# Performance work log

Hardware: AMD Instinct MI355X
Metric: run time of the kernel (lower is better)

Reference implementation:

```python
import jax, jax.numpy as jnp
import numpy as np

ALPHA = 1.0
BETA = 10.0
MARGIN = 0.5


def setup_inputs() -> dict:
    key = jax.random.key(0)
    k1, k2 = jax.random.split(key)
    emb = jax.random.normal(k1, (4096, 512), dtype=jnp.float32)
    # module docstring: embeddings are L2-normalized
    emb = emb / jnp.linalg.norm(emb, axis=1, keepdims=True)
    labels = jax.random.randint(k2, (4096,), 0, 64, dtype=jnp.int64)
    return {"embeddings": emb, "labels": labels}


def reference(embeddings, labels):
    n = embeddings.shape[0]
    sim = embeddings @ embeddings.T  # [n, n]
    labels_eq = labels[None, :] == labels[:, None]
    eye = jnp.eye(n, dtype=bool)
    pos_mask = labels_eq & ~eye
    neg_mask = ~labels_eq & ~eye

    # masked exp-sums (masked entries contribute 0, matching torch's
    # clone/NEG_INF/zero-out dance without materializing extra copies)
    pos_exp = jnp.where(pos_mask, jnp.exp(-ALPHA * (sim - MARGIN)), 0.0)
    neg_exp = jnp.where(neg_mask, jnp.exp(BETA * (sim - MARGIN)), 0.0)
    pos_term = (1.0 / ALPHA) * jnp.log1p(pos_exp.sum(axis=1))
    neg_term = (1.0 / BETA) * jnp.log1p(neg_exp.sum(axis=1))

    valid = pos_mask.any(axis=1) & neg_mask.any(axis=1)
    n_valid = valid.sum()
    total = jnp.where(valid, pos_term + neg_term, 0.0).sum()
    return jnp.where(n_valid > 0, total / jnp.maximum(n_valid, 1).astype(sim.dtype), 0.0)
```

## Files before the change

### kernel.cpp

```cpp
#include <hip/hip_runtime.h>
#include <hip/hip_bf16.h>

#define N 4096
#define D 512
#define MARGIN 0.5f
#define BETA 10.0f

typedef __attribute__((ext_vector_type(8))) short short8;
typedef __attribute__((ext_vector_type(4))) float floatx4;

__device__ inline unsigned short f2bf(float f) {
    unsigned u = __float_as_uint(f);
    u += 0x7fffu + ((u >> 16) & 1u);
    return (unsigned short)(u >> 16);
}

#define GLOAD_LDS16(gp, lp)                                             \
    __builtin_amdgcn_global_load_lds(                                   \
        (const __attribute__((address_space(1))) void*)(gp),            \
        (__attribute__((address_space(3))) void*)(lp), 16, 0, 0)

__global__ __launch_bounds__(256) void convert_bf16_kernel(
        const float4* __restrict__ in, ushort4* __restrict__ out,
        float* __restrict__ sums ) {
    int idx = blockIdx.x * 256 + threadIdx.x;
    if (idx < 2 * N) sums[idx] = 0.f;
    float4 v = in[idx];
    ushort4 o;
    o.x = f2bf(v.x); o.y = f2bf(v.y); o.z = f2bf(v.z); o.w = f2bf(v.w);
    out[idx] = o;
}

__global__ __launch_bounds__(256, 4) void ms_loss_gemm(
        const unsigned short* __restrict__ Ebf,
        const int* __restrict__ labels,
        float* __restrict__ pos_sum,
        float* __restrict__ neg_sum) {
    __shared__ char Als[64 * 256];
    __shared__ char Bls[64 * 256];
    __shared__ int rlab[64];
    __shared__ int clab[64];

    int t = blockIdx.x;
    int bi = 0;
    while (t >= (64 - bi)) { t -= (64 - bi); ++bi; }
    const int bj = bi + t;
    const bool diag = (bi == bj);

    const int tid  = threadIdx.x;
    const int wave = tid >> 6;
    const int lane = tid & 63;
    const int quad = lane >> 4;
    const int lcol = lane & 15;
    const int wrow = wave >> 1;
    const int wcol = wave & 1;
    const int ibase = bi * 64;
    const int jbase = bj * 64;

    if (tid < 64)        rlab[tid]      = labels[ibase + tid];
    else if (tid < 128)  clab[tid - 64] = labels[jbase + tid - 64];

    floatx4 acc[2][2];
#pragma unroll
    for (int mt = 0; mt < 2; ++mt)
#pragma unroll
        for (int nt = 0; nt < 2; ++nt)
            acc[mt][nt] = (floatx4){0.f, 0.f, 0.f, 0.f};

    const char* Eb = (const char*)Ebf;
    const int srow = lane >> 4;
    const int sgrp = wave * 4 + srow;
    const int sck  = ((lane & 15) ^ sgrp) * 16;
    const size_t aoff0 = (size_t)(ibase + sgrp) * 1024 + sck;
    const size_t boff0 = (size_t)(jbase + sgrp) * 1024 + sck;
    const int ldso = wave * 1024 + lane * 16;

#define STAGE(kt_)                                                         \
    {                                                                      \
        const int kb_ = (kt_) * 256;                                       \
        _Pragma("unroll")                                                  \
        for (int it = 0; it < 4; ++it) {                                   \
            GLOAD_LDS16(Eb + aoff0 + (size_t)it * 16384 + kb_,             \
                        Als + ldso + it * 4096);                           \
            if (!diag)                                                     \
                GLOAD_LDS16(Eb + boff0 + (size_t)it * 16384 + kb_,         \
                            Bls + ldso + it * 4096);                       \
        }                                                                  \
    }

#pragma unroll
    for (int kt = 0; kt < D / 128; ++kt) {
        __syncthreads();
        STAGE(kt);
        __syncthreads();

        const char* Ac = Als;
        const char* Bc = diag ? Als : Bls;
#pragma unroll
        for (int s = 0; s < 4; ++s) {
            short8 a[2], b[2];
            const int rslot = ((s * 4 + quad) ^ lcol) * 16;
#pragma unroll
            for (int mt = 0; mt < 2; ++mt) {
                int r = wrow * 32 + mt * 16 + lcol;
                a[mt] = *(const short8*)(Ac + r * 256 + rslot);
            }
#pragma unroll
            for (int nt = 0; nt < 2; ++nt) {
                int c = wcol * 32 + nt * 16 + lcol;
                b[nt] = *(const short8*)(Bc + c * 256 + rslot);
            }
#pragma unroll
            for (int mt = 0; mt < 2; ++mt)
#pragma unroll
                for (int nt = 0; nt < 2; ++nt)
                    acc[mt][nt] = __builtin_amdgcn_mfma_f32_16x16x32_bf16(
                        a[mt], b[nt], acc[mt][nt], 0, 0, 0);
        }
    }

    int ljv[2], gjv[2];
#pragma unroll
    for (int nt = 0; nt < 2; ++nt) {
        int cl = wcol * 32 + nt * 16 + lcol;
        ljv[nt] = clab[cl];
        gjv[nt] = jbase + cl;
    }

    float colp[2] = {0.f, 0.f};
    float coln[2] = {0.f, 0.f};

#pragma unroll
    for (int mt = 0; mt < 2; ++mt) {
#pragma unroll
        for (int reg = 0; reg < 4; ++reg) {
            int rl = wrow * 32 + mt * 16 + quad * 4 + reg;
            int gi = ibase + rl;
            int li = rlab[rl];
            float p = 0.f, ng = 0.f;
#pragma unroll
            for (int nt = 0; nt < 2; ++nt) {
                float s = acc[mt][nt][reg];
                if (gi != gjv[nt]) {
                    if (li == ljv[nt]) {
                        float e = __expf(MARGIN - s);
                        p += e;  colp[nt] += e;
                    } else {
                        float e = __expf(BETA * (s - MARGIN));
                        ng += e; coln[nt] += e;
                    }
                }
            }
            p  += __shfl_xor(p, 1);   ng += __shfl_xor(ng, 1);
            p  += __shfl_xor(p, 2);   ng += __shfl_xor(ng, 2);
            p  += __shfl_xor(p, 4);   ng += __shfl_xor(ng, 4);
            p  += __shfl_xor(p, 8);   ng += __shfl_xor(ng, 8);
            if (lcol == 0) {
                atomicAdd(&pos_sum[gi], p);
                atomicAdd(&neg_sum[gi], ng);
            }
        }
    }

    if (!diag) {
#pragma unroll
        for (int nt = 0; nt < 2; ++nt) {
            float cp = colp[nt], cn = coln[nt];
            cp += __shfl_xor(cp, 16);  cn += __shfl_xor(cn, 16);
            cp += __shfl_xor(cp, 32);  cn += __shfl_xor(cn, 32);
            if (quad == 0) {
                int gj = gjv[nt];
                atomicAdd(&pos_sum[gj], cp);
                atomicAdd(&neg_sum[gj], cn);
            }
        }
    }
}

__global__ __launch_bounds__(256) void finalize_kernel(
        const float4* __restrict__ pos4, const float4* __restrict__ neg4,
        float* __restrict__ out) {
    __shared__ float sb[256];
    __shared__ int   sc[256];
    const int tid = threadIdx.x;
    float tot = 0.f;
    int cnt = 0;
#pragma unroll
    for (int it = 0; it < N / 4 / 256; ++it) {
        int i = it * 256 + tid;
        float4 p = pos4[i];
        float4 ng = neg4[i];
        const float* pp = (const float*)&p;
        const float* nn = (const float*)&ng;
#pragma unroll
        for (int j = 0; j < 4; ++j) {
            if (pp[j] > 0.f && nn[j] > 0.f) {
                tot += log1pf(pp[j]) + (1.0f / BETA) * log1pf(nn[j]);
                cnt += 1;
            }
        }
    }
    sb[tid] = tot; sc[tid] = cnt;
    __syncthreads();
    for (int s = 128; s > 0; s >>= 1) {
        if (tid < s) { sb[tid] += sb[tid + s]; sc[tid] += sc[tid + s]; }
        __syncthreads();
    }
    if (tid == 0) out[0] = (sc[0] > 0) ? sb[0] / (float)sc[0] : 0.f;
}

extern "C" void kernel_launch(void* const* d_in, const int* in_sizes, int n_in,
                              void* d_out, int out_size, void* d_ws, size_t ws_size,
                              hipStream_t stream) {
    const float* emb   = (const float*)d_in[0];
    const int* labels  = (const int*)d_in[1];
    float* out         = (float*)d_out;

    char* ws = (char*)d_ws;
    unsigned short* Ebf = (unsigned short*)ws;
    float* pos_sum = (float*)(ws + (size_t)N * D * 2);
    float* neg_sum = pos_sum + N;

    convert_bf16_kernel<<<(N * D / 4) / 256, 256, 0, stream>>>(
        (const float4*)emb, (ushort4*)Ebf, pos_sum);

    ms_loss_gemm<<<(64 * 65) / 2, 256, 0, stream>>>(Ebf, labels, pos_sum, neg_sum);

    finalize_kernel<<<1, 256, 0, stream>>>(
        (const float4*)pos_sum, (const float4*)neg_sum, out);
}
```

Before: 104.9 us.

## Use 128x64 output tiles over 128-row block triangle with 64-wide K steps

Each workgroup now computes a 128-row by 64-column tile: it takes a 128x128 upper-triangular block pair and splits the columns into two halves across workgroups. The K step per stage drops from 128 to 64 so the larger A tile still fits in LDS, and the XOR swizzle is adjusted to the 128-byte row. Each B fragment now feeds twice as many MFMAs, which raises arithmetic intensity and halves the grid size. The cost is more sync/load rounds per tile, double the accumulator registers, and no A/B LDS sharing on diagonal tiles.

```diff
diff --git a/kernel.cpp b/kernel.cpp
--- a/kernel.cpp
+++ b/kernel.cpp
@@ -36,15 +36,17 @@
         const int* __restrict__ labels,
         float* __restrict__ pos_sum,
         float* __restrict__ neg_sum) {
-    __shared__ char Als[64 * 256];
-    __shared__ char Bls[64 * 256];
-    __shared__ int rlab[64];
+    __shared__ char Als[128 * 128];
+    __shared__ char Bls[64 * 128];
+    __shared__ int rlab[128];
     __shared__ int clab[64];
 
     int t = blockIdx.x;
+    const int h = t & 1;
+    int pr = t >> 1;
     int bi = 0;
-    while (t >= (64 - bi)) { t -= (64 - bi); ++bi; }
-    const int bj = bi + t;
+    while (pr >= (32 - bi)) { pr -= (32 - bi); ++bi; }
+    const int bj = bi + pr;
     const bool diag = (bi == bj);
 
     const int tid  = threadIdx.x;
@@ -54,64 +56,63 @@
     const int lcol = lane & 15;
     const int wrow = wave >> 1;
     const int wcol = wave & 1;
-    const int ibase = bi * 64;
-    const int jbase = bj * 64;
-
-    if (tid < 64)        rlab[tid]      = labels[ibase + tid];
-    else if (tid < 128)  clab[tid - 64] = labels[jbase + tid - 64];
-
-    floatx4 acc[2][2];
-#pragma unroll
-    for (int mt = 0; mt < 2; ++mt)
+    const int ibase = bi * 128;
+    const int jbase = bj * 128 + h * 64;
+
+    if (tid < 128)       rlab[tid]       = labels[ibase + tid];
+    else if (tid < 192)  clab[tid - 128] = labels[jbase + tid - 128];
+
+    floatx4 acc[4][2];
+#pragma unroll
+    for (int mt = 0; mt < 4; ++mt)
 #pragma unroll
         for (int nt = 0; nt < 2; ++nt)
             acc[mt][nt] = (floatx4){0.f, 0.f, 0.f, 0.f};
 
     const char* Eb = (const char*)Ebf;
-    const int srow = lane >> 4;
-    const int sgrp = wave * 4 + srow;
-    const int sck  = ((lane & 15) ^ sgrp) * 16;
-    const size_t aoff0 = (size_t)(ibase + sgrp) * 1024 + sck;
-    const size_t boff0 = (size_t)(jbase + sgrp) * 1024 + sck;
+    const int srow8 = lane >> 3;
+    const int sck   = ((lane & 7) ^ srow8) * 16;
+    const size_t aoff0 = (size_t)(ibase + wave * 8 + srow8) * 1024 + sck;
+    const size_t boff0 = (size_t)(jbase + wave * 8 + srow8) * 1024 + sck;
     const int ldso = wave * 1024 + lane * 16;
 
 #define STAGE(kt_)                                                         \
     {                                                                      \
-        const int kb_ = (kt_) * 256;                                       \
+        const int kb_ = (kt_) * 128;                                       \
         _Pragma("unroll")                                                  \
-        for (int it = 0; it < 4; ++it) {                                   \
-            GLOAD_LDS16(Eb + aoff0 + (size_t)it * 16384 + kb_,             \
+        for (int it = 0; it < 4; ++it)                                     \
+            GLOAD_LDS16(Eb + aoff0 + (size_t)it * 32768 + kb_,             \
                         Als + ldso + it * 4096);                           \
-            if (!diag)                                                     \
-                GLOAD_LDS16(Eb + boff0 + (size_t)it * 16384 + kb_,         \
-                            Bls + ldso + it * 4096);                       \
-        }                                                                  \
-    }
-
-#pragma unroll
-    for (int kt = 0; kt < D / 128; ++kt) {
+        _Pragma("unroll")                                                  \
+        for (int it = 0; it < 2; ++it)                                     \
+            GLOAD_LDS16(Eb + boff0 + (size_t)it * 32768 + kb_,             \
+                        Bls + ldso + it * 4096);                           \
+    }
+
+    const int rsw = lcol & 7;
+
+#pragma unroll
+    for (int kt = 0; kt < D / 64; ++kt) {
         __syncthreads();
         STAGE(kt);
         __syncthreads();
 
-        const char* Ac = Als;
-        const char* Bc = diag ? Als : Bls;
-#pragma unroll
-        for (int s = 0; s < 4; ++s) {
-            short8 a[2], b[2];
-            const int rslot = ((s * 4 + quad) ^ lcol) * 16;
-#pragma unroll
-            for (int mt = 0; mt < 2; ++mt) {
-                int r = wrow * 32 + mt * 16 + lcol;
-                a[mt] = *(const short8*)(Ac + r * 256 + rslot);
+#pragma unroll
+        for (int s = 0; s < 2; ++s) {
+            short8 a[4], b[2];
+            const int rslot = ((s * 4 + quad) ^ rsw) * 16;
+#pragma unroll
+            for (int mt = 0; mt < 4; ++mt) {
+                int r = wrow * 64 + mt * 16 + lcol;
+                a[mt] = *(const short8*)(Als + r * 128 + rslot);
             }
 #pragma unroll
             for (int nt = 0; nt < 2; ++nt) {
                 int c = wcol * 32 + nt * 16 + lcol;
-                b[nt] = *(const short8*)(Bc + c * 256 + rslot);
-            }
-#pragma unroll
-            for (int mt = 0; mt < 2; ++mt)
+                b[nt] = *(const short8*)(Bls + c * 128 + rslot);
+            }
+#pragma unroll
+            for (int mt = 0; mt < 4; ++mt)
 #pragma unroll
                 for (int nt = 0; nt < 2; ++nt)
                     acc[mt][nt] = __builtin_amdgcn_mfma_f32_16x16x32_bf16(
@@ -131,10 +132,10 @@
     float coln[2] = {0.f, 0.f};
 
 #pragma unroll
-    for (int mt = 0; mt < 2; ++mt) {
+    for (int mt = 0; mt < 4; ++mt) {
 #pragma unroll
         for (int reg = 0; reg < 4; ++reg) {
-            int rl = wrow * 32 + mt * 16 + quad * 4 + reg;
+            int rl = wrow * 64 + mt * 16 + quad * 4 + reg;
             int gi = ibase + rl;
             int li = rlab[rl];
             float p = 0.f, ng = 0.f;
@@ -224,7 +225,8 @@
     convert_bf16_kernel<<<(N * D / 4) / 256, 256, 0, stream>>>(
         (const float4*)emb, (ushort4*)Ebf, pos_sum);
 
-    ms_loss_gemm<<<(64 * 65) / 2, 256, 0, stream>>>(Ebf, labels, pos_sum, neg_sum);
+    ms_loss_gemm<<<(32 * 33) / 2 * 2, 256, 0, stream>>>(
+        Ebf, labels, pos_sum, neg_sum);
 
     finalize_kernel<<<1, 256, 0, stream>>>(
         (const float4*)pos_sum, (const float4*)neg_sum, out);
```

Result: faster. 101.2 us (-3.5%).
